# Optimization experiments

Hardware: AMD Instinct MI355X
Metric: run time of the kernel (lower is better)

Reference implementation:

```python
import jax, jax.numpy as jnp
import numpy as np

SEQ, B, IN, H = 512, 64, 256, 512

def _lin_params(key, out_d, in_d):
    k1, k2 = jax.random.split(key)
    bound = 1.0 / np.sqrt(in_d)
    w = jax.random.uniform(k1, (out_d, in_d), jnp.float32, -bound, bound)
    b = jax.random.uniform(k2, (out_d,), jnp.float32, -bound, bound)
    return w, b

def setup_inputs() -> dict:
    key = jax.random.key(0)
    ks = jax.random.split(key, 9)
    x = jax.random.normal(ks[0], (SEQ, B, IN), jnp.float32)
    h0 = jnp.zeros((B, H), jnp.float32)
    c0 = jnp.zeros((B, H), jnp.float32)
    Wf_w, Wf_b = _lin_params(ks[1], H, IN)
    Uf_w, Uf_b = _lin_params(ks[2], H, H)
    Wi_w, Wi_b = _lin_params(ks[3], H, IN)
    Ui_w, Ui_b = _lin_params(ks[4], H, H)
    Wo_w, Wo_b = _lin_params(ks[5], H, IN)
    Uo_w, Uo_b = _lin_params(ks[6], H, H)
    Wc_w, Wc_b = _lin_params(ks[7], H, IN)
    Uc_w, Uc_b = _lin_params(ks[8], H, H)
    return dict(x=x, h0=h0, c0=c0,
                Wf_w=Wf_w, Wf_b=Wf_b, Uf_w=Uf_w, Uf_b=Uf_b,
                Wi_w=Wi_w, Wi_b=Wi_b, Ui_w=Ui_w, Ui_b=Ui_b,
                Wo_w=Wo_w, Wo_b=Wo_b, Uo_w=Uo_w, Uo_b=Uo_b,
                Wc_w=Wc_w, Wc_b=Wc_b, Uc_w=Uc_w, Uc_b=Uc_b)

def reference(x, h0, c0,
              Wf_w, Wf_b, Uf_w, Uf_b,
              Wi_w, Wi_b, Ui_w, Ui_b,
              Wo_w, Wo_b, Uo_w, Uo_b,
              Wc_w, Wc_b, Uc_w, Uc_b):
    # Precompute all input-to-hidden projections in one batched GEMM per gate.
    xf = jnp.einsum('tbi,hi->tbh', x, Wf_w) + Wf_b  # (T,B,H)
    xi = jnp.einsum('tbi,hi->tbh', x, Wi_w) + Wi_b
    xo = jnp.einsum('tbi,hi->tbh', x, Wo_w) + Wo_b
    xc = jnp.einsum('tbi,hi->tbh', x, Wc_w) + Wc_b

    def step(carry, xs):
        h, c = carry
        xft, xit, xot, xct = xs
        f = jax.nn.sigmoid(xft + h @ Uf_w.T + Uf_b)
        i = jax.nn.sigmoid(xit + h @ Ui_w.T + Ui_b)
        o = jax.nn.sigmoid(xot + h @ Uo_w.T + Uo_b)
        c = f * c + i * jnp.tanh(xct + h @ Uc_w.T + Uc_b)
        h = o * jnp.tanh(c)
        return (h, c), h

    (h, c), h_seq = jax.lax.scan(step, (h0, c0), (xf, xi, xo, xc))
    return h_seq, h, c
```

## Files before the change

### kernel.cpp

```cpp
#include <hip/hip_runtime.h>


#define T_STEPS 512
#define BATCH   64
#define IN_D    256
#define HID     512
#define NGROUP  4
#define NSLICE  16
#define BLK_B   16
#define BLK_H   32
#define THREADS 512
#define CH_ROW  128
#define SLOT_BYTES (NGROUP * BLK_B * CH_ROW * 16)
#define EXCH_INTS  (2 * SLOT_BYTES / 4)

using short8  = __attribute__((ext_vector_type(8))) short;
using int4v   = __attribute__((ext_vector_type(4))) int;
using float4v = __attribute__((ext_vector_type(4))) float;

#define FRAG_ADDR(f) (((f) << 4) + (((f) >> 4) << 4))

__device__ __forceinline__ unsigned short f2bf(float f) {
    union { float f; unsigned int i; } v; v.f = f;
    unsigned int r = v.i + 0x7fff + ((v.i >> 16) & 1);
    return (unsigned short)(r >> 16);
}
__device__ __forceinline__ short8 pack8(float4 a, float4 b) {
    short8 s;
    s[0]=(short)f2bf(a.x); s[1]=(short)f2bf(a.y); s[2]=(short)f2bf(a.z); s[3]=(short)f2bf(a.w);
    s[4]=(short)f2bf(b.x); s[5]=(short)f2bf(b.y); s[6]=(short)f2bf(b.z); s[7]=(short)f2bf(b.w);
    return s;
}
__device__ __forceinline__ float sigm(float v) { return 1.0f / (1.0f + __expf(-v)); }
__device__ __forceinline__ float tanh_(float v) { return 2.0f / (1.0f + __expf(-2.0f * v)) - 1.0f; }

__device__ __forceinline__ void lds_barrier() {
    asm volatile("s_waitcnt lgkmcnt(0)" ::: "memory");
    __builtin_amdgcn_s_barrier();
    __builtin_amdgcn_sched_barrier(0);
}

__global__ __launch_bounds__(256, 1) void lstm_init_ws(unsigned int* w, int n) {
    int i = blockIdx.x * blockDim.x + threadIdx.x;
    if (i < n) __hip_atomic_store(&w[i], 0u, __ATOMIC_RELAXED, __HIP_MEMORY_SCOPE_AGENT);
}

__global__ __launch_bounds__(THREADS, 1) void lstm_persist(
    const float* __restrict__ x,
    const float* __restrict__ h0,
    const float* __restrict__ c0,
    const float* __restrict__ Wf, const float* __restrict__ Wfb,
    const float* __restrict__ Uf, const float* __restrict__ Ufb,
    const float* __restrict__ Wi, const float* __restrict__ Wib,
    const float* __restrict__ Ui, const float* __restrict__ Uib,
    const float* __restrict__ Wo, const float* __restrict__ Wob,
    const float* __restrict__ Uo, const float* __restrict__ Uob,
    const float* __restrict__ Wc, const float* __restrict__ Wcb,
    const float* __restrict__ Uc, const float* __restrict__ Ucb,
    float* out,
    unsigned char* exch)
{
    __shared__ __attribute__((aligned(16))) unsigned char hfrag[17392];
    __shared__ __attribute__((aligned(16))) unsigned char xfrag[8688];
    __shared__ float g_lds[8 * 256];

    const int tid  = threadIdx.x;
    const int lane = tid & 63;
    const int wave = tid >> 6;
    const int gate = wave >> 1;
    const int hlf  = wave & 1;
    const int grp  = blockIdx.x & 3;
    const int slc  = blockIdx.x >> 2;
    const int bb   = grp * BLK_B;
    const int hbase= slc * BLK_H;
    const int lm   = lane & 15;
    const int lq   = lane >> 4;
    const int row  = tid >> 5;
    const int seg  = tid & 31;

    const float* Ug  = (gate == 0) ? Uf : (gate == 1) ? Ui : (gate == 2) ? Uo : Uc;
    const float* Wg  = (gate == 0) ? Wf : (gate == 1) ? Wi : (gate == 2) ? Wo : Wc;
    const float* Wbg = (gate == 0) ? Wfb : (gate == 1) ? Wib : (gate == 2) ? Wob : Wcb;
    const float* Ubg = (gate == 0) ? Ufb : (gate == 1) ? Uib : (gate == 2) ? Uob : Ucb;
    const int ng = hbase + hlf * 16 + lm;

    short8 ufrag[16];
#pragma unroll
    for (int ks = 0; ks < 16; ++ks) {
        const float* p = Ug + (size_t)ng * HID + ks * 32 + lq * 8;
        ufrag[ks] = pack8(*(const float4*)(p), *(const float4*)(p + 4));
    }
    short8 wfrag[8];
#pragma unroll
    for (int ks = 0; ks < 8; ++ks) {
        const float* p = Wg + (size_t)ng * IN_D + ks * 32 + lq * 8;
        wfrag[ks] = pack8(*(const float4*)(p), *(const float4*)(p + 4));
    }
    const float bias = Wbg[ng] + Ubg[ng];

    float c_reg = c0[(size_t)(bb + row) * HID + hbase + seg];

    {
        const float* ph = h0 + (size_t)(bb + row) * HID + seg * 16;
        int f0 = (seg >> 1) * 64 + (seg & 1) * 32 + row;
        *(short8*)(hfrag + FRAG_ADDR(f0))      = pack8(*(const float4*)(ph),     *(const float4*)(ph + 4));
        *(short8*)(hfrag + FRAG_ADDR(f0 + 16)) = pack8(*(const float4*)(ph + 8), *(const float4*)(ph + 12));

        const float* px = x + (size_t)(bb + row) * IN_D + seg * 8;
        int fx = (seg >> 2) * 64 + (seg & 3) * 16 + row;
        *(short8*)(xfrag + FRAG_ADDR(fx)) = pack8(*(const float4*)(px), *(const float4*)(px + 4));
    }
    float4 xn0, xn1;
    {
        const float* px = x + ((size_t)1 * BATCH + bb + row) * IN_D + seg * 8;
        xn0 = *(const float4*)(px); xn1 = *(const float4*)(px + 4);
    }
    __syncthreads();

    float4v accx0 = {bias, bias, bias, bias};
    float4v accx1 = {0.f, 0.f, 0.f, 0.f};
#pragma unroll
    for (int ks = 0; ks < 8; ++ks) {
        short8 a = *(const short8*)(xfrag + FRAG_ADDR(ks * 64 + lane));
        if (ks & 1) accx1 = __builtin_amdgcn_mfma_f32_16x16x32_bf16(a, wfrag[ks], accx1, 0, 0, 0);
        else        accx0 = __builtin_amdgcn_mfma_f32_16x16x32_bf16(a, wfrag[ks], accx0, 0, 0, 0);
    }

    float* const out_h = out + (size_t)T_STEPS * BATCH * HID;
    float* const out_c = out_h + (size_t)BATCH * HID;

    unsigned char* const ex_wr = exch
        + (size_t)((grp * BLK_B + row) * CH_ROW + slc * 8 + (seg >> 2)) * 16;
    unsigned char* const ex_rd = exch
        + (size_t)((grp * BLK_B + row) * CH_ROW + seg * 4) * 16;

    for (int t = 0; t < T_STEPS; ++t) {
        float4 xm0, xm1;
        {
            int tn = (t + 2 < T_STEPS) ? (t + 2) : (T_STEPS - 1);
            const float* px = x + ((size_t)tn * BATCH + bb + row) * IN_D + seg * 8;
            xm0 = *(const float4*)(px); xm1 = *(const float4*)(px + 4);
        }

        float4v acc0 = accx0, acc1 = accx1;
#pragma unroll
        for (int ks = 0; ks < 16; ++ks) {
            short8 a = *(const short8*)(hfrag + FRAG_ADDR(ks * 64 + lane));
            if (ks & 1) acc1 = __builtin_amdgcn_mfma_f32_16x16x32_bf16(a, ufrag[ks], acc1, 0, 0, 0);
            else        acc0 = __builtin_amdgcn_mfma_f32_16x16x32_bf16(a, ufrag[ks], acc0, 0, 0, 0);
        }
        float4v acc = acc0 + acc1;
#pragma unroll
        for (int r = 0; r < 4; ++r)
            g_lds[wave * 256 + (lq * 4 + r) * 16 + lm] = acc[r];

        if (t + 1 < T_STEPS) {
            int fx = (seg >> 2) * 64 + (seg & 3) * 16 + row;
            *(short8*)(xfrag + FRAG_ADDR(fx)) = pack8(xn0, xn1);
            xn0 = xm0; xn1 = xm1;
        }

        lds_barrier();

        float hv;
        {
            int hf2 = seg >> 4, nn = seg & 15;
            float fpre = g_lds[(0 * 2 + hf2) * 256 + row * 16 + nn];
            float ipre = g_lds[(1 * 2 + hf2) * 256 + row * 16 + nn];
            float opre = g_lds[(2 * 2 + hf2) * 256 + row * 16 + nn];
            float gpre = g_lds[(3 * 2 + hf2) * 256 + row * 16 + nn];
            float fv = sigm(fpre), iv = sigm(ipre), ov = sigm(opre);
            float gv = tanh_(gpre);
            c_reg = fv * c_reg + iv * gv;
            hv = ov * tanh_(c_reg);
        }
        out[((size_t)t * BATCH + bb + row) * HID + hbase + seg] = hv;

        if (t + 1 < T_STEPS) {
            {
                unsigned int bfv = f2bf(hv);
                unsigned int nb  = (unsigned int)__shfl_xor((int)bfv, 1);
                unsigned int p   = bfv | (nb << 16);
                unsigned int q   = (unsigned int)__shfl_xor((int)p, 2);
                if ((lane & 3) == 0) {
                    int4v ch; ch[0] = (int)p; ch[1] = (int)q; ch[2] = t + 1; ch[3] = 0;
                    const unsigned char* pa = ex_wr + (size_t)(t & 1) * SLOT_BYTES;
                    asm volatile("global_store_dwordx4 %0, %1, off sc0 sc1"
                                 :: "v"(pa), "v"(ch) : "memory");
                }
            }

            accx0 = (float4v){bias, bias, bias, bias};
            accx1 = (float4v){0.f, 0.f, 0.f, 0.f};
#pragma unroll
            for (int ks = 0; ks < 8; ++ks) {
                short8 a = *(const short8*)(xfrag + FRAG_ADDR(ks * 64 + lane));
                if (ks & 1) accx1 = __builtin_amdgcn_mfma_f32_16x16x32_bf16(a, wfrag[ks], accx1, 0, 0, 0);
                else        accx0 = __builtin_amdgcn_mfma_f32_16x16x32_bf16(a, wfrag[ks], accx0, 0, 0, 0);
            }

            const unsigned char* pb = ex_rd + (size_t)(t & 1) * SLOT_BYTES;
            const int want = t + 1;
            int4v e0, e1, e2, e3;
            int guard = 0;
            for (;;) {
                asm volatile(
                    "global_load_dwordx4 %0, %4, off sc0 sc1\n\t"
                    "global_load_dwordx4 %1, %4, off offset:16 sc0 sc1\n\t"
                    "global_load_dwordx4 %2, %4, off offset:32 sc0 sc1\n\t"
                    "global_load_dwordx4 %3, %4, off offset:48 sc0 sc1\n\t"
                    "s_waitcnt vmcnt(0)"
                    : "=&v"(e0), "=&v"(e1), "=&v"(e2), "=&v"(e3)
                    : "v"(pb) : "memory");
                if ((e0[2] == want) & (e1[2] == want) & (e2[2] == want) & (e3[2] == want)) break;
                if (++guard > (1 << 20)) break;
            }
            int f0 = (seg >> 1) * 64 + (seg & 1) * 32 + row;
            int4v d0 = {e0[0], e0[1], e1[0], e1[1]};
            int4v d1 = {e2[0], e2[1], e3[0], e3[1]};
            *(int4v*)(hfrag + FRAG_ADDR(f0))      = d0;
            *(int4v*)(hfrag + FRAG_ADDR(f0 + 16)) = d1;

            lds_barrier();
        } else {
            out_h[(size_t)(bb + row) * HID + hbase + seg] = hv;
            out_c[(size_t)(bb + row) * HID + hbase + seg] = c_reg;
        }
    }
}

extern "C" void kernel_launch(void* const* d_in, const int* in_sizes, int n_in,
                              void* d_out, int out_size, void* d_ws, size_t ws_size,
                              hipStream_t stream) {
    (void)in_sizes; (void)n_in; (void)out_size; (void)ws_size;
    const float* x   = (const float*)d_in[0];
    const float* h0  = (const float*)d_in[1];
    const float* c0  = (const float*)d_in[2];
    const float* Wf  = (const float*)d_in[3];
    const float* Wfb = (const float*)d_in[4];
    const float* Uf  = (const float*)d_in[5];
    const float* Ufb = (const float*)d_in[6];
    const float* Wi  = (const float*)d_in[7];
    const float* Wib = (const float*)d_in[8];
    const float* Ui  = (const float*)d_in[9];
    const float* Uib = (const float*)d_in[10];
    const float* Wo  = (const float*)d_in[11];
    const float* Wob = (const float*)d_in[12];
    const float* Uo  = (const float*)d_in[13];
    const float* Uob = (const float*)d_in[14];
    const float* Wc  = (const float*)d_in[15];
    const float* Wcb = (const float*)d_in[16];
    const float* Uc  = (const float*)d_in[17];
    const float* Ucb = (const float*)d_in[18];

    unsigned int* ws = (unsigned int*)d_ws;
    lstm_init_ws<<<(EXCH_INTS + 255) / 256, 256, 0, stream>>>(ws, EXCH_INTS);
    lstm_persist<<<NGROUP * NSLICE, THREADS, 0, stream>>>(
        x, h0, c0,
        Wf, Wfb, Uf, Ufb, Wi, Wib, Ui, Uib,
        Wo, Wob, Uo, Uob, Wc, Wcb, Uc, Ucb,
        (float*)d_out, (unsigned char*)d_ws);
}
```

Baseline: 1.785 ms.

## Double grid to 128 blocks and add adaptive fast/slow cache-scope exchange path

Splits the batch into 8 groups of 8 rows, so 128 persistent blocks run with half the batch rows each (the upper half of each MFMA tile is zero padding). The hidden-state exchange gains a fast path that stores and loads with sc0 only instead of sc0 sc1. A warmup of 8 steps probes whether that path delivers data within a bounded number of polls, and a grid-wide vote then selects fast or fully coherent exchange for the remaining steps. The step loop is also unrolled by two to ping-pong the x prefetch registers. The fast path relies on cache-coherence behaviour seen during warmup, and half the MFMA work is wasted on padded rows.

```diff
diff --git a/kernel.cpp b/kernel.cpp
--- a/kernel.cpp
+++ b/kernel.cpp
@@ -5,14 +5,16 @@
 #define BATCH   64
 #define IN_D    256
 #define HID     512
-#define NGROUP  4
+#define NGROUP  8
 #define NSLICE  16
-#define BLK_B   16
+#define BLK_B   8
 #define BLK_H   32
 #define THREADS 512
+#define NBLK    (NGROUP * NSLICE)
 #define CH_ROW  128
 #define SLOT_BYTES (NGROUP * BLK_B * CH_ROW * 16)
-#define EXCH_INTS  (2 * SLOT_BYTES / 4)
+#define WARMUP   8
+#define FAST_CAP 128
 
 using short8  = __attribute__((ext_vector_type(8))) short;
 using int4v   = __attribute__((ext_vector_type(4))) int;
@@ -58,25 +60,31 @@
     const float* __restrict__ Wc, const float* __restrict__ Wcb,
     const float* __restrict__ Uc, const float* __restrict__ Ucb,
     float* out,
-    unsigned char* exch)
+    unsigned char* ex_fast,
+    unsigned char* ex_slow,
+    unsigned int* ctrl)
 {
     __shared__ __attribute__((aligned(16))) unsigned char hfrag[17392];
     __shared__ __attribute__((aligned(16))) unsigned char xfrag[8688];
-    __shared__ float g_lds[8 * 256];
+    __shared__ float g_lds[8 * 320];
+    __shared__ unsigned int warm_fail_lds;
+    __shared__ unsigned int mode_lds;
 
     const int tid  = threadIdx.x;
     const int lane = tid & 63;
     const int wave = tid >> 6;
     const int gate = wave >> 1;
     const int hlf  = wave & 1;
-    const int grp  = blockIdx.x & 3;
-    const int slc  = blockIdx.x >> 2;
+    const int grp  = blockIdx.x & 7;
+    const int slc  = blockIdx.x >> 3;
     const int bb   = grp * BLK_B;
     const int hbase= slc * BLK_H;
     const int lm   = lane & 15;
     const int lq   = lane >> 4;
     const int row  = tid >> 5;
     const int seg  = tid & 31;
+    const int pr   = tid & 7;
+    const int kb   = tid >> 3;
 
     const float* Ug  = (gate == 0) ? Uf : (gate == 1) ? Ui : (gate == 2) ? Uo : Uc;
     const float* Wg  = (gate == 0) ? Wf : (gate == 1) ? Wi : (gate == 2) ? Wo : Wc;
@@ -98,22 +106,27 @@
     }
     const float bias = Wbg[ng] + Ubg[ng];
 
-    float c_reg = c0[(size_t)(bb + row) * HID + hbase + seg];
-
-    {
+    for (int i = tid; i < 17392 / 4; i += THREADS) ((unsigned int*)hfrag)[i] = 0u;
+    for (int i = tid; i < 8688 / 4;  i += THREADS) ((unsigned int*)xfrag)[i] = 0u;
+    if (tid == 0) { warm_fail_lds = 0u; mode_lds = 0u; }
+    __syncthreads();
+
+    float c_reg = 0.f;
+    if (row < 8) c_reg = c0[(size_t)(bb + row) * HID + hbase + seg];
+
+    if (row < 8) {
         const float* ph = h0 + (size_t)(bb + row) * HID + seg * 16;
         int f0 = (seg >> 1) * 64 + (seg & 1) * 32 + row;
         *(short8*)(hfrag + FRAG_ADDR(f0))      = pack8(*(const float4*)(ph),     *(const float4*)(ph + 4));
         *(short8*)(hfrag + FRAG_ADDR(f0 + 16)) = pack8(*(const float4*)(ph + 8), *(const float4*)(ph + 12));
-
         const float* px = x + (size_t)(bb + row) * IN_D + seg * 8;
         int fx = (seg >> 2) * 64 + (seg & 3) * 16 + row;
         *(short8*)(xfrag + FRAG_ADDR(fx)) = pack8(*(const float4*)(px), *(const float4*)(px + 4));
     }
-    float4 xn0, xn1;
-    {
+    float4 xa0 = {0,0,0,0}, xa1 = {0,0,0,0}, xb0 = {0,0,0,0}, xb1 = {0,0,0,0};
+    if (row < 8) {
         const float* px = x + ((size_t)1 * BATCH + bb + row) * IN_D + seg * 8;
-        xn0 = *(const float4*)(px); xn1 = *(const float4*)(px + 4);
+        xa0 = *(const float4*)(px); xa1 = *(const float4*)(px + 4);
     }
     __syncthreads();
 
@@ -129,17 +142,34 @@
     float* const out_h = out + (size_t)T_STEPS * BATCH * HID;
     float* const out_c = out_h + (size_t)BATCH * HID;
 
-    unsigned char* const ex_wr = exch
-        + (size_t)((grp * BLK_B + row) * CH_ROW + slc * 8 + (seg >> 2)) * 16;
-    unsigned char* const ex_rd = exch
-        + (size_t)((grp * BLK_B + row) * CH_ROW + seg * 4) * 16;
-
-    for (int t = 0; t < T_STEPS; ++t) {
-        float4 xm0, xm1;
-        {
+    unsigned char* const fa_wr = ex_fast + (size_t)((bb + row) * CH_ROW + slc * 8 + (seg >> 2)) * 16;
+    unsigned char* const sl_wr = ex_slow + (size_t)((bb + row) * CH_ROW + slc * 8 + (seg >> 2)) * 16;
+    const unsigned char* const fa_rd = ex_fast + (size_t)((bb + pr) * CH_ROW + kb * 2) * 16;
+    const unsigned char* const sl_rd = ex_slow + (size_t)((bb + pr) * CH_ROW + kb * 2) * 16;
+
+    int mode = 0;
+
+    auto STEP = [&](int t, float4& sx0, float4& sx1, float4& px0, float4& px1) {
+        if (t == WARMUP) {
+            if (tid == 0) {
+                if (warm_fail_lds)
+                    __hip_atomic_store(&ctrl[0], 1u, __ATOMIC_RELAXED, __HIP_MEMORY_SCOPE_AGENT);
+                asm volatile("s_waitcnt vmcnt(0)" ::: "memory");
+                __hip_atomic_fetch_add(&ctrl[1], 1u, __ATOMIC_RELAXED, __HIP_MEMORY_SCOPE_AGENT);
+                long g = 0;
+                while (__hip_atomic_load(&ctrl[1], __ATOMIC_RELAXED, __HIP_MEMORY_SCOPE_AGENT) < (unsigned)NBLK
+                       && ++g < (1L << 26)) { }
+                mode_lds = __hip_atomic_load(&ctrl[0], __ATOMIC_RELAXED, __HIP_MEMORY_SCOPE_AGENT);
+            }
+            __syncthreads();
+            mode = (int)mode_lds;
+        }
+        const bool warm = (t < WARMUP);
+
+        if (row < 8) {
             int tn = (t + 2 < T_STEPS) ? (t + 2) : (T_STEPS - 1);
             const float* px = x + ((size_t)tn * BATCH + bb + row) * IN_D + seg * 8;
-            xm0 = *(const float4*)(px); xm1 = *(const float4*)(px + 4);
+            px0 = *(const float4*)(px); px1 = *(const float4*)(px + 4);
         }
 
         float4v acc0 = accx0, acc1 = accx1;
@@ -152,41 +182,45 @@
         float4v acc = acc0 + acc1;
 #pragma unroll
         for (int r = 0; r < 4; ++r)
-            g_lds[wave * 256 + (lq * 4 + r) * 16 + lm] = acc[r];
-
-        if (t + 1 < T_STEPS) {
+            g_lds[wave * 320 + lq * 80 + r * 16 + lm] = acc[r];
+
+        if (t + 1 < T_STEPS && row < 8) {
             int fx = (seg >> 2) * 64 + (seg & 3) * 16 + row;
-            *(short8*)(xfrag + FRAG_ADDR(fx)) = pack8(xn0, xn1);
-            xn0 = xm0; xn1 = xm1;
+            *(short8*)(xfrag + FRAG_ADDR(fx)) = pack8(sx0, sx1);
         }
 
         lds_barrier();
 
-        float hv;
-        {
+        float hv = 0.f;
+        if (row < 8) {
             int hf2 = seg >> 4, nn = seg & 15;
-            float fpre = g_lds[(0 * 2 + hf2) * 256 + row * 16 + nn];
-            float ipre = g_lds[(1 * 2 + hf2) * 256 + row * 16 + nn];
-            float opre = g_lds[(2 * 2 + hf2) * 256 + row * 16 + nn];
-            float gpre = g_lds[(3 * 2 + hf2) * 256 + row * 16 + nn];
+            int rbase = (row >> 2) * 80 + (row & 3) * 16 + nn;
+            float fpre = g_lds[(0 * 2 + hf2) * 320 + rbase];
+            float ipre = g_lds[(1 * 2 + hf2) * 320 + rbase];
+            float opre = g_lds[(2 * 2 + hf2) * 320 + rbase];
+            float gpre = g_lds[(3 * 2 + hf2) * 320 + rbase];
             float fv = sigm(fpre), iv = sigm(ipre), ov = sigm(opre);
             float gv = tanh_(gpre);
             c_reg = fv * c_reg + iv * gv;
             hv = ov * tanh_(c_reg);
-        }
-        out[((size_t)t * BATCH + bb + row) * HID + hbase + seg] = hv;
+            out[((size_t)t * BATCH + bb + row) * HID + hbase + seg] = hv;
+        }
 
         if (t + 1 < T_STEPS) {
-            {
+            if (row < 8) {
                 unsigned int bfv = f2bf(hv);
                 unsigned int nb  = (unsigned int)__shfl_xor((int)bfv, 1);
                 unsigned int p   = bfv | (nb << 16);
                 unsigned int q   = (unsigned int)__shfl_xor((int)p, 2);
-                if ((lane & 3) == 0) {
+                if ((tid & 3) == 0) {
                     int4v ch; ch[0] = (int)p; ch[1] = (int)q; ch[2] = t + 1; ch[3] = 0;
-                    const unsigned char* pa = ex_wr + (size_t)(t & 1) * SLOT_BYTES;
-                    asm volatile("global_store_dwordx4 %0, %1, off sc0 sc1"
-                                 :: "v"(pa), "v"(ch) : "memory");
+                    const size_t so = (size_t)(t & 1) * SLOT_BYTES;
+                    if (warm || mode == 0)
+                        asm volatile("global_store_dwordx4 %0, %1, off sc0"
+                                     :: "v"(fa_wr + so), "v"(ch) : "memory");
+                    if (warm || mode == 1)
+                        asm volatile("global_store_dwordx4 %0, %1, off sc0 sc1"
+                                     :: "v"(sl_wr + so), "v"(ch) : "memory");
                 }
             }
 
@@ -199,40 +233,58 @@
                 else        accx0 = __builtin_amdgcn_mfma_f32_16x16x32_bf16(a, wfrag[ks], accx0, 0, 0, 0);
             }
 
-            const unsigned char* pb = ex_rd + (size_t)(t & 1) * SLOT_BYTES;
             const int want = t + 1;
-            int4v e0, e1, e2, e3;
-            int guard = 0;
-            for (;;) {
-                asm volatile(
-                    "global_load_dwordx4 %0, %4, off sc0 sc1\n\t"
-                    "global_load_dwordx4 %1, %4, off offset:16 sc0 sc1\n\t"
-                    "global_load_dwordx4 %2, %4, off offset:32 sc0 sc1\n\t"
-                    "global_load_dwordx4 %3, %4, off offset:48 sc0 sc1\n\t"
-                    "s_waitcnt vmcnt(0)"
-                    : "=&v"(e0), "=&v"(e1), "=&v"(e2), "=&v"(e3)
-                    : "v"(pb) : "memory");
-                if ((e0[2] == want) & (e1[2] == want) & (e2[2] == want) & (e3[2] == want)) break;
-                if (++guard > (1 << 20)) break;
-            }
-            int f0 = (seg >> 1) * 64 + (seg & 1) * 32 + row;
-            int4v d0 = {e0[0], e0[1], e1[0], e1[1]};
-            int4v d1 = {e2[0], e2[1], e3[0], e3[1]};
-            *(int4v*)(hfrag + FRAG_ADDR(f0))      = d0;
-            *(int4v*)(hfrag + FRAG_ADDR(f0 + 16)) = d1;
+            const size_t so = (size_t)(t & 1) * SLOT_BYTES;
+            int4v e0, e1;
+            bool got = false;
+            if (warm || mode == 0) {
+                const unsigned char* pb = fa_rd + so;
+                long cap = warm ? (long)FAST_CAP : (1L << 24);
+                for (long it = 0; it < cap; ++it) {
+                    asm volatile(
+                        "global_load_dwordx4 %0, %2, off sc0\n\t"
+                        "global_load_dwordx4 %1, %2, off offset:16 sc0\n\t"
+                        "s_waitcnt vmcnt(0)"
+                        : "=&v"(e0), "=&v"(e1) : "v"(pb) : "memory");
+                    if ((e0[2] == want) & (e1[2] == want)) { got = true; break; }
+                }
+            }
+            if (!got) {
+                if (warm) warm_fail_lds = 1u;
+                const unsigned char* pb = sl_rd + so;
+                long guard = 0;
+                for (;;) {
+                    asm volatile(
+                        "global_load_dwordx4 %0, %2, off sc0 sc1\n\t"
+                        "global_load_dwordx4 %1, %2, off offset:16 sc0 sc1\n\t"
+                        "s_waitcnt vmcnt(0)"
+                        : "=&v"(e0), "=&v"(e1) : "v"(pb) : "memory");
+                    if ((e0[2] == want) & (e1[2] == want)) break;
+                    if (++guard > (1L << 24)) break;
+                }
+            }
+            int f0 = (kb >> 2) * 64 + (kb & 3) * 16 + pr;
+            *(int4v*)(hfrag + FRAG_ADDR(f0)) = (int4v){e0[0], e0[1], e1[0], e1[1]};
 
             lds_barrier();
         } else {
-            out_h[(size_t)(bb + row) * HID + hbase + seg] = hv;
-            out_c[(size_t)(bb + row) * HID + hbase + seg] = c_reg;
-        }
+            if (row < 8) {
+                out_h[(size_t)(bb + row) * HID + hbase + seg] = hv;
+                out_c[(size_t)(bb + row) * HID + hbase + seg] = c_reg;
+            }
+        }
+    };
+
+    for (int t = 0; t < T_STEPS; t += 2) {
+        STEP(t,     xa0, xa1, xb0, xb1);
+        STEP(t + 1, xb0, xb1, xa0, xa1);
     }
 }
 
 extern "C" void kernel_launch(void* const* d_in, const int* in_sizes, int n_in,
                               void* d_out, int out_size, void* d_ws, size_t ws_size,
                               hipStream_t stream) {
-    (void)in_sizes; (void)n_in; (void)out_size; (void)ws_size;
+    (void)in_sizes; (void)n_in; (void)out_size;
     const float* x   = (const float*)d_in[0];
     const float* h0  = (const float*)d_in[1];
     const float* c0  = (const float*)d_in[2];
@@ -253,11 +305,24 @@
     const float* Uc  = (const float*)d_in[17];
     const float* Ucb = (const float*)d_in[18];
 
-    unsigned int* ws = (unsigned int*)d_ws;
-    lstm_init_ws<<<(EXCH_INTS + 255) / 256, 256, 0, stream>>>(ws, EXCH_INTS);
-    lstm_persist<<<NGROUP * NSLICE, THREADS, 0, stream>>>(
+    unsigned char* base = (unsigned char*)d_ws;
+    unsigned char* ex_fast = base;
+    unsigned char* ex_slow;
+    size_t used;
+    if (ws_size >= 4 * (size_t)SLOT_BYTES + 64) {
+        ex_slow = base + 2 * (size_t)SLOT_BYTES;
+        used = 4 * (size_t)SLOT_BYTES + 64;
+    } else {
+        ex_slow = base;
+        used = 2 * (size_t)SLOT_BYTES + 64;
+    }
+    unsigned int* ctrl = (unsigned int*)(base + used - 64);
+
+    const int nzero = (int)(used / 4);
+    lstm_init_ws<<<(nzero + 255) / 256, 256, 0, stream>>>((unsigned int*)base, nzero);
+    lstm_persist<<<NBLK, THREADS, 0, stream>>>(
         x, h0, c0,
         Wf, Wfb, Uf, Ufb, Wi, Wib, Ui, Uib,
         Wo, Wob, Uo, Uob, Wc, Wcb, Uc, Ucb,
-        (float*)d_out, (unsigned char*)d_ws);
-}
+        (float*)d_out, ex_fast, ex_slow, ctrl);
+}
```

Result: slower. 1.827 ms (+2.4%).

## Replace per-chunk tagged h exchange with packed payload plus per-block flags

Applied to the files above, without the earlier changes.

Replaces the exchange of hidden state between blocks. Before, each 16-byte chunk carried a step tag and every thread polled its own chunks. Now h is written as compact bf16 pairs and each block, after a barrier, publishes a single step flag; one thread polls the group's 16 flags, then every thread loads its payload once. The timestep loop is also unrolled by two so the x prefetch registers ping-pong instead of being copied. This cuts exchange bandwidth and polling traffic but adds two block barriers and a serial flag publish-then-poll on each step's critical path.

```diff
diff --git a/kernel.cpp b/kernel.cpp
--- a/kernel.cpp
+++ b/kernel.cpp
@@ -10,9 +10,11 @@
 #define BLK_B   16
 #define BLK_H   32
 #define THREADS 512
-#define CH_ROW  128
-#define SLOT_BYTES (NGROUP * BLK_B * CH_ROW * 16)
-#define EXCH_INTS  (2 * SLOT_BYTES / 4)
+#define ROW_BYTES  1024
+#define GRP_BYTES  (BLK_B * ROW_BYTES)
+#define SLOT_BYTES (NGROUP * GRP_BYTES)
+#define FLAGS_OFF  (2 * SLOT_BYTES)
+#define NFLAGS     (NGROUP * NSLICE)
 
 using short8  = __attribute__((ext_vector_type(8))) short;
 using int4v   = __attribute__((ext_vector_type(4))) int;
@@ -110,10 +112,10 @@
         int fx = (seg >> 2) * 64 + (seg & 3) * 16 + row;
         *(short8*)(xfrag + FRAG_ADDR(fx)) = pack8(*(const float4*)(px), *(const float4*)(px + 4));
     }
-    float4 xn0, xn1;
+    float4 xa0, xa1, xb0 = {0,0,0,0}, xb1 = {0,0,0,0};
     {
         const float* px = x + ((size_t)1 * BATCH + bb + row) * IN_D + seg * 8;
-        xn0 = *(const float4*)(px); xn1 = *(const float4*)(px + 4);
+        xa0 = *(const float4*)(px); xa1 = *(const float4*)(px + 4);
     }
     __syncthreads();
 
@@ -129,19 +131,13 @@
     float* const out_h = out + (size_t)T_STEPS * BATCH * HID;
     float* const out_c = out_h + (size_t)BATCH * HID;
 
-    unsigned char* const ex_wr = exch
-        + (size_t)((grp * BLK_B + row) * CH_ROW + slc * 8 + (seg >> 2)) * 16;
-    unsigned char* const ex_rd = exch
-        + (size_t)((grp * BLK_B + row) * CH_ROW + seg * 4) * 16;
-
-    for (int t = 0; t < T_STEPS; ++t) {
-        float4 xm0, xm1;
-        {
-            int tn = (t + 2 < T_STEPS) ? (t + 2) : (T_STEPS - 1);
-            const float* px = x + ((size_t)tn * BATCH + bb + row) * IN_D + seg * 8;
-            xm0 = *(const float4*)(px); xm1 = *(const float4*)(px + 4);
-        }
-
+    unsigned char* const ex_wr = exch + (size_t)grp * GRP_BYTES
+                               + (size_t)row * ROW_BYTES + (size_t)(hbase + seg) * 2;
+    const unsigned char* const ex_rd = exch + (size_t)grp * GRP_BYTES + (size_t)tid * 32;
+    unsigned int* const flg = (unsigned int*)(exch + FLAGS_OFF) + grp * NSLICE;
+    unsigned int* const flg_wr = flg + slc;
+
+    auto STEP = [&](int t, float4& sx0, float4& sx1, float4& px0, float4& px1) {
         float4v acc0 = accx0, acc1 = accx1;
 #pragma unroll
         for (int ks = 0; ks < 16; ++ks) {
@@ -156,8 +152,7 @@
 
         if (t + 1 < T_STEPS) {
             int fx = (seg >> 2) * 64 + (seg & 3) * 16 + row;
-            *(short8*)(xfrag + FRAG_ADDR(fx)) = pack8(xn0, xn1);
-            xn0 = xm0; xn1 = xm1;
+            *(short8*)(xfrag + FRAG_ADDR(fx)) = pack8(sx0, sx1);
         }
 
         lds_barrier();
@@ -180,14 +175,25 @@
             {
                 unsigned int bfv = f2bf(hv);
                 unsigned int nb  = (unsigned int)__shfl_xor((int)bfv, 1);
-                unsigned int p   = bfv | (nb << 16);
-                unsigned int q   = (unsigned int)__shfl_xor((int)p, 2);
-                if ((lane & 3) == 0) {
-                    int4v ch; ch[0] = (int)p; ch[1] = (int)q; ch[2] = t + 1; ch[3] = 0;
+                if ((tid & 1) == 0) {
+                    unsigned int pw = bfv | (nb << 16);
                     const unsigned char* pa = ex_wr + (size_t)(t & 1) * SLOT_BYTES;
-                    asm volatile("global_store_dwordx4 %0, %1, off sc0 sc1"
-                                 :: "v"(pa), "v"(ch) : "memory");
+                    asm volatile("global_store_dword %0, %1, off sc0 sc1"
+                                 :: "v"(pa), "v"(pw) : "memory");
                 }
+            }
+            asm volatile("s_waitcnt vmcnt(0)" ::: "memory");
+            __builtin_amdgcn_s_barrier();
+            __builtin_amdgcn_sched_barrier(0);
+            if (tid == 0) {
+                asm volatile("global_store_dword %0, %1, off sc0 sc1"
+                             :: "v"(flg_wr), "v"((unsigned int)(t + 1)) : "memory");
+            }
+
+            {
+                int tn = (t + 2 < T_STEPS) ? (t + 2) : (T_STEPS - 1);
+                const float* px = x + ((size_t)tn * BATCH + bb + row) * IN_D + seg * 8;
+                px0 = *(const float4*)(px); px1 = *(const float4*)(px + 4);
             }
 
             accx0 = (float4v){bias, bias, bias, bias};
@@ -199,33 +205,56 @@
                 else        accx0 = __builtin_amdgcn_mfma_f32_16x16x32_bf16(a, wfrag[ks], accx0, 0, 0, 0);
             }
 
-            const unsigned char* pb = ex_rd + (size_t)(t & 1) * SLOT_BYTES;
-            const int want = t + 1;
-            int4v e0, e1, e2, e3;
-            int guard = 0;
-            for (;;) {
+            if (tid == 0) {
+                const unsigned int want = (unsigned int)(t + 1);
+                int4v q0, q1, q2, q3;
+                long guard = 0;
+                for (;;) {
+                    asm volatile(
+                        "global_load_dwordx4 %0, %4, off sc0 sc1\n\t"
+                        "global_load_dwordx4 %1, %4, off offset:16 sc0 sc1\n\t"
+                        "global_load_dwordx4 %2, %4, off offset:32 sc0 sc1\n\t"
+                        "global_load_dwordx4 %3, %4, off offset:48 sc0 sc1\n\t"
+                        "s_waitcnt vmcnt(0)"
+                        : "=&v"(q0), "=&v"(q1), "=&v"(q2), "=&v"(q3)
+                        : "v"(flg) : "memory");
+                    bool ok = true;
+#pragma unroll
+                    for (int j = 0; j < 4; ++j) {
+                        ok &= ((unsigned int)q0[j] >= want);
+                        ok &= ((unsigned int)q1[j] >= want);
+                        ok &= ((unsigned int)q2[j] >= want);
+                        ok &= ((unsigned int)q3[j] >= want);
+                    }
+                    if (ok) break;
+                    if (++guard > (1L << 22)) break;
+                }
+            }
+            __builtin_amdgcn_s_barrier();
+            __builtin_amdgcn_sched_barrier(0);
+
+            {
+                const unsigned char* pb = ex_rd + (size_t)(t & 1) * SLOT_BYTES;
+                int4v e0, e1;
                 asm volatile(
-                    "global_load_dwordx4 %0, %4, off sc0 sc1\n\t"
-                    "global_load_dwordx4 %1, %4, off offset:16 sc0 sc1\n\t"
-                    "global_load_dwordx4 %2, %4, off offset:32 sc0 sc1\n\t"
-                    "global_load_dwordx4 %3, %4, off offset:48 sc0 sc1\n\t"
+                    "global_load_dwordx4 %0, %2, off sc0 sc1\n\t"
+                    "global_load_dwordx4 %1, %2, off offset:16 sc0 sc1\n\t"
                     "s_waitcnt vmcnt(0)"
-                    : "=&v"(e0), "=&v"(e1), "=&v"(e2), "=&v"(e3)
-                    : "v"(pb) : "memory");
-                if ((e0[2] == want) & (e1[2] == want) & (e2[2] == want) & (e3[2] == want)) break;
-                if (++guard > (1 << 20)) break;
-            }
-            int f0 = (seg >> 1) * 64 + (seg & 1) * 32 + row;
-            int4v d0 = {e0[0], e0[1], e1[0], e1[1]};
-            int4v d1 = {e2[0], e2[1], e3[0], e3[1]};
-            *(int4v*)(hfrag + FRAG_ADDR(f0))      = d0;
-            *(int4v*)(hfrag + FRAG_ADDR(f0 + 16)) = d1;
-
+                    : "=&v"(e0), "=&v"(e1) : "v"(pb) : "memory");
+                int f0 = (seg >> 1) * 64 + (seg & 1) * 32 + row;
+                *(int4v*)(hfrag + FRAG_ADDR(f0))      = e0;
+                *(int4v*)(hfrag + FRAG_ADDR(f0 + 16)) = e1;
+            }
             lds_barrier();
         } else {
             out_h[(size_t)(bb + row) * HID + hbase + seg] = hv;
             out_c[(size_t)(bb + row) * HID + hbase + seg] = c_reg;
         }
+    };
+
+    for (int t = 0; t < T_STEPS; t += 2) {
+        STEP(t,     xa0, xa1, xb0, xb1);
+        STEP(t + 1, xb0, xb1, xa0, xa1);
     }
 }
 
@@ -253,11 +282,12 @@
     const float* Uc  = (const float*)d_in[17];
     const float* Ucb = (const float*)d_in[18];
 
-    unsigned int* ws = (unsigned int*)d_ws;
-    lstm_init_ws<<<(EXCH_INTS + 255) / 256, 256, 0, stream>>>(ws, EXCH_INTS);
+    unsigned char* exch = (unsigned char*)d_ws;
+    unsigned int* flags = (unsigned int*)(exch + FLAGS_OFF);
+    lstm_init_ws<<<1, 256, 0, stream>>>(flags, NFLAGS);
     lstm_persist<<<NGROUP * NSLICE, THREADS, 0, stream>>>(
         x, h0, c0,
         Wf, Wfb, Uf, Ufb, Wi, Wib, Ui, Uib,
         Wo, Wob, Uo, Uob, Wc, Wcb, Uc, Ucb,
-        (float*)d_out, (unsigned char*)d_ws);
-}
+        (float*)d_out, exch);
+}
```

After: 1.532 ms. -14.1%, faster.
